# Kernel optimization log

Measured on AMD Instinct MI355X. Metric: run time of the kernel, lower is better.

The kernel has to match this reference:

```python
import jax, jax.numpy as jnp
import numpy as np

FACTOR = 0.5  # matches init_kwargs factor


def setup_inputs() -> dict:
    key = jax.random.key(0)
    k1, k2 = jax.random.split(key)
    E, D, N = 1600000, 32, 100000
    edge_data = jax.random.normal(k1, (E, D), dtype=jnp.float32)
    edge_dst = jax.random.randint(k2, (E,), 0, N, dtype=jnp.int64)
    return {"edge_data": edge_data, "edge_dst": edge_dst, "num_nodes": N}


def reference(edge_data, edge_dst, num_nodes):
    # EdgewiseReduce.forward: optional scalar premultiply, then scatter-sum
    # edge features into per-node bins by destination index.
    scaled = edge_data * FACTOR                     # [E, D]
    out = jax.ops.segment_sum(scaled, edge_dst, num_segments=num_nodes)  # [N, D]
    return out
```

## Files before the change

### kernel.cpp

```cpp
#include <hip/hip_runtime.h>
#include <hip/hip_bf16.h>


#define D 32
#define FACTOR 0.5f
#define BSHIFT 7
#define BNODES (1 << BSHIFT)
#define CAPSHIFT 12
#define CAP (1 << CAPSHIFT)

__global__ void init_kernel(int* __restrict__ cursor, int* __restrict__ ovf_count,
                            int nb) {
  int i = blockIdx.x * blockDim.x + threadIdx.x;
  if (i == 0) *ovf_count = 0;
  if (i < nb) cursor[i] = i << CAPSHIFT;
}

__global__ void scatter_kernel(const int* __restrict__ dst, int* __restrict__ gcursor,
                               int* __restrict__ order, int2* __restrict__ ovf,
                               int* __restrict__ ovf_count, int E, int N, int nb,
                               int chunk) {
  extern __shared__ int sm[];
  int* lhist = sm;
  int* lcur = sm + nb;
  int lo = blockIdx.x * chunk;
  int hiE = min(lo + chunk, E);
  const int4* dst4 = (const int4*)dst;

  for (int i = threadIdx.x; i < nb; i += blockDim.x) lhist[i] = 0;
  __syncthreads();

  int lo4 = lo >> 2;
  int full4 = (hiE - lo) >> 2;
  for (int i = threadIdx.x; i < full4; i += blockDim.x) {
    int4 v = dst4[lo4 + i];
    if ((unsigned)v.x < (unsigned)N) atomicAdd(&lhist[v.x >> BSHIFT], 1);
    if ((unsigned)v.y < (unsigned)N) atomicAdd(&lhist[v.y >> BSHIFT], 1);
    if ((unsigned)v.z < (unsigned)N) atomicAdd(&lhist[v.z >> BSHIFT], 1);
    if ((unsigned)v.w < (unsigned)N) atomicAdd(&lhist[v.w >> BSHIFT], 1);
  }
  int tb = lo + (full4 << 2) + threadIdx.x;
  if (tb < hiE) {
    int d = dst[tb];
    if ((unsigned)d < (unsigned)N) atomicAdd(&lhist[d >> BSHIFT], 1);
  }
  __syncthreads();

  for (int i = threadIdx.x; i < nb; i += blockDim.x) {
    int c = lhist[i];
    lcur[i] = c ? atomicAdd(&gcursor[i], c) : 0;
  }
  __syncthreads();

  #define EMIT(dd, ee)                                                        \
    if ((unsigned)(dd) < (unsigned)N) {                                       \
      int bkt = (dd) >> BSHIFT;                                               \
      int pos = atomicAdd(&lcur[bkt], 1);                                     \
      if (pos < ((bkt + 1) << CAPSHIFT)) {                                    \
        order[pos] = ((ee) << BSHIFT) | ((dd) & (BNODES - 1));                \
      } else {                                                                \
        int op = atomicAdd(ovf_count, 1);                                     \
        ovf[op] = make_int2((ee), (dd));                                      \
      }                                                                       \
    }

  for (int i = threadIdx.x; i < full4; i += blockDim.x) {
    int e = lo + (i << 2);
    int4 v = dst4[lo4 + i];
    EMIT(v.x, e + 0)
    EMIT(v.y, e + 1)
    EMIT(v.z, e + 2)
    EMIT(v.w, e + 3)
  }
  if (tb < hiE) {
    int d = dst[tb];
    EMIT(d, tb)
  }
  #undef EMIT
}

#define K4_THREADS 512
__global__ __launch_bounds__(K4_THREADS)
void gather_kernel(const float4* __restrict__ data, const int* __restrict__ order,
                   const int* __restrict__ cursor, float4* __restrict__ out,
                   int N) {
  __shared__ int ids[CAP];
  __shared__ int sorted[CAP];
  __shared__ int hist[BNODES];
  __shared__ int offs[BNODES];
  __shared__ int cur[BNODES];

  const int b = blockIdx.x;
  const int base = b << CAPSHIFT;
  int cnt = cursor[b] - base;
  if (cnt > CAP) cnt = CAP;
  const int lo = b << BSHIFT;
  const int tid = threadIdx.x;
  const int grp = tid >> 2;
  const int ln = tid & 3;

  for (int i = tid; i < BNODES; i += K4_THREADS) hist[i] = 0;
  __syncthreads();
  for (int i = tid; i < cnt; i += K4_THREADS) {
    int v = order[base + i];
    ids[i] = v;
    atomicAdd(&hist[v & (BNODES - 1)], 1);
  }
  __syncthreads();

  if (tid < 64) {
    int c0 = hist[2 * tid], c1 = hist[2 * tid + 1];
    int s = c0 + c1;
    int sc = s;
    #pragma unroll
    for (int off = 1; off < 64; off <<= 1) {
      int t = __shfl_up(sc, off);
      if (tid >= off) sc += t;
    }
    int bs = sc - s;
    offs[2 * tid] = bs + c0;
    offs[2 * tid + 1] = bs + c0 + c1;
    cur[2 * tid] = bs;
    cur[2 * tid + 1] = bs + c0;
  }
  __syncthreads();

  for (int i = tid; i < cnt; i += K4_THREADS) {
    int v = ids[i];
    sorted[atomicAdd(&cur[v & (BNODES - 1)], 1)] = v;
  }
  __syncthreads();

  float4 acc0 = make_float4(0.f, 0.f, 0.f, 0.f);
  float4 acc1 = make_float4(0.f, 0.f, 0.f, 0.f);
  int e_ = offs[grp];
  int i = e_ - hist[grp];
  for (; i + 3 < e_; i += 4) {
    int r0 = sorted[i] >> BSHIFT;
    int r1 = sorted[i + 1] >> BSHIFT;
    int r2 = sorted[i + 2] >> BSHIFT;
    int r3 = sorted[i + 3] >> BSHIFT;
    const float4* p0 = data + (size_t)r0 * 8 + ln * 2;
    const float4* p1 = data + (size_t)r1 * 8 + ln * 2;
    const float4* p2 = data + (size_t)r2 * 8 + ln * 2;
    const float4* p3 = data + (size_t)r3 * 8 + ln * 2;
    float4 x0 = p0[0], y0 = p0[1];
    float4 x1 = p1[0], y1 = p1[1];
    float4 x2 = p2[0], y2 = p2[1];
    float4 x3 = p3[0], y3 = p3[1];
    acc0.x += x0.x + x1.x + x2.x + x3.x;
    acc0.y += x0.y + x1.y + x2.y + x3.y;
    acc0.z += x0.z + x1.z + x2.z + x3.z;
    acc0.w += x0.w + x1.w + x2.w + x3.w;
    acc1.x += y0.x + y1.x + y2.x + y3.x;
    acc1.y += y0.y + y1.y + y2.y + y3.y;
    acc1.z += y0.z + y1.z + y2.z + y3.z;
    acc1.w += y0.w + y1.w + y2.w + y3.w;
  }
  for (; i < e_; ++i) {
    int r0 = sorted[i] >> BSHIFT;
    const float4* p0 = data + (size_t)r0 * 8 + ln * 2;
    float4 x0 = p0[0], y0 = p0[1];
    acc0.x += x0.x; acc0.y += x0.y; acc0.z += x0.z; acc0.w += x0.w;
    acc1.x += y0.x; acc1.y += y0.y; acc1.z += y0.z; acc1.w += y0.w;
  }

  int node = lo + grp;
  if (node < N) {
    float4 o0, o1;
    o0.x = acc0.x * FACTOR; o0.y = acc0.y * FACTOR;
    o0.z = acc0.z * FACTOR; o0.w = acc0.w * FACTOR;
    o1.x = acc1.x * FACTOR; o1.y = acc1.y * FACTOR;
    o1.z = acc1.z * FACTOR; o1.w = acc1.w * FACTOR;
    out[(size_t)node * 8 + ln * 2] = o0;
    out[(size_t)node * 8 + ln * 2 + 1] = o1;
  }
}

__global__ void overflow_kernel(const float4* __restrict__ data,
                                const int2* __restrict__ ovf,
                                const int* __restrict__ ovf_count,
                                float* __restrict__ out) {
  int cnt = *ovf_count;
  for (int i = blockIdx.x * blockDim.x + threadIdx.x; i < cnt * 8;
       i += gridDim.x * blockDim.x) {
    int k = i >> 3, q = i & 7;
    int2 ed = ovf[k];
    float4 v = data[(size_t)ed.x * 8 + q];
    float* p = out + (size_t)ed.y * D + q * 4;
    unsafeAtomicAdd(p + 0, v.x * FACTOR);
    unsafeAtomicAdd(p + 1, v.y * FACTOR);
    unsafeAtomicAdd(p + 2, v.z * FACTOR);
    unsafeAtomicAdd(p + 3, v.w * FACTOR);
  }
}

__global__ void atomic_kernel(const float4* __restrict__ edge_data,
                              const int* __restrict__ edge_dst,
                              float* __restrict__ out, int E, int N) {
  int tid = blockIdx.x * blockDim.x + threadIdx.x;
  int e = tid >> 3;
  int q = tid & 7;
  if (e >= E) return;
  int dst = edge_dst[e];
  if (dst < 0 || dst >= N) return;
  float4 v = edge_data[(size_t)e * 8 + q];
  float* p = out + (size_t)dst * D + q * 4;
  unsafeAtomicAdd(p + 0, v.x * FACTOR);
  unsafeAtomicAdd(p + 1, v.y * FACTOR);
  unsafeAtomicAdd(p + 2, v.z * FACTOR);
  unsafeAtomicAdd(p + 3, v.w * FACTOR);
}

extern "C" void kernel_launch(void* const* d_in, const int* in_sizes, int n_in,
                              void* d_out, int out_size, void* d_ws, size_t ws_size,
                              hipStream_t stream) {
  const float4* edge_data = (const float4*)d_in[0];
  const int* edge_dst = (const int*)d_in[1];

  int E = in_sizes[1];
  int N = out_size / D;

  int nb = (N + BNODES - 1) >> BSHIFT;
  size_t ofs_order = 4 + (size_t)nb;
  ofs_order = (ofs_order + 1) & ~(size_t)1;
  size_t ofs_ovf = ofs_order + (size_t)nb * CAP;
  ofs_ovf = (ofs_ovf + 1) & ~(size_t)1;
  size_t need = (ofs_ovf + (size_t)2 * E) * sizeof(int);
  bool pack_ok = ((long long)E << BSHIFT) < (1ll << 31) &&
                 (((long long)nb << CAPSHIFT) < (1ll << 31));

  if (ws_size < need || !pack_ok) {
    float* out = (float*)d_out;
    hipMemsetAsync(d_out, 0, (size_t)out_size * sizeof(float), stream);
    int total = E * 8;
    atomic_kernel<<<(total + 255) / 256, 256, 0, stream>>>(edge_data, edge_dst, out, E, N);
    return;
  }

  int* ws = (int*)d_ws;
  int* ovf_count = ws;
  int* cursor = ws + 4;
  int* order = ws + ofs_order;
  int2* ovf = (int2*)(ws + ofs_ovf);

  init_kernel<<<(nb + 1023) / 1024, 1024, 0, stream>>>(cursor, ovf_count, nb);

  int nblk = 128;
  int chunk = ((E + nblk - 1) / nblk + 3) & ~3;
  size_t lds = (size_t)2 * nb * sizeof(int);
  scatter_kernel<<<nblk, 256, lds, stream>>>(edge_dst, cursor, order, ovf,
                                             ovf_count, E, N, nb, chunk);

  gather_kernel<<<nb, K4_THREADS, 0, stream>>>(
      edge_data, order, cursor, (float4*)d_out, N);

  overflow_kernel<<<32, 256, 0, stream>>>(edge_data, ovf, ovf_count, (float*)d_out);
}
```

Baseline: 329.7 us.

## Balance gather work by splitting sorted edges evenly across groups with LDS flush

The gather kernel now gives each 4-thread group an equal contiguous slice of the bucket's sorted edge list instead of one node's edges. Partial sums are flushed into a shared-memory accumulator with LDS atomics at node boundaries, and the result is then scaled and written out. This targets load imbalance from varying node degrees within a block. In exchange it adds LDS atomics, extra per-edge boundary checks and another barrier, and it reuses the ids buffer as the accumulator.

```diff
diff --git a/kernel.cpp b/kernel.cpp
--- a/kernel.cpp
+++ b/kernel.cpp
@@ -84,16 +84,17 @@
 void gather_kernel(const float4* __restrict__ data, const int* __restrict__ order,
                    const int* __restrict__ cursor, float4* __restrict__ out,
                    int N) {
+  __shared__ int sorted[CAP];
   __shared__ int ids[CAP];
-  __shared__ int sorted[CAP];
   __shared__ int hist[BNODES];
-  __shared__ int offs[BNODES];
+  __shared__ int endo[BNODES];
   __shared__ int cur[BNODES];
 
   const int b = blockIdx.x;
   const int base = b << CAPSHIFT;
   int cnt = cursor[b] - base;
   if (cnt > CAP) cnt = CAP;
+  if (cnt < 0) cnt = 0;
   const int lo = b << BSHIFT;
   const int tid = threadIdx.x;
   const int grp = tid >> 2;
@@ -118,8 +119,8 @@
       if (tid >= off) sc += t;
     }
     int bs = sc - s;
-    offs[2 * tid] = bs + c0;
-    offs[2 * tid + 1] = bs + c0 + c1;
+    endo[2 * tid] = bs + c0;
+    endo[2 * tid + 1] = bs + c0 + c1;
     cur[2 * tid] = bs;
     cur[2 * tid + 1] = bs + c0;
   }
@@ -131,49 +132,75 @@
   }
   __syncthreads();
 
-  float4 acc0 = make_float4(0.f, 0.f, 0.f, 0.f);
-  float4 acc1 = make_float4(0.f, 0.f, 0.f, 0.f);
-  int e_ = offs[grp];
-  int i = e_ - hist[grp];
-  for (; i + 3 < e_; i += 4) {
-    int r0 = sorted[i] >> BSHIFT;
-    int r1 = sorted[i + 1] >> BSHIFT;
-    int r2 = sorted[i + 2] >> BSHIFT;
-    int r3 = sorted[i + 3] >> BSHIFT;
-    const float4* p0 = data + (size_t)r0 * 8 + ln * 2;
-    const float4* p1 = data + (size_t)r1 * 8 + ln * 2;
-    const float4* p2 = data + (size_t)r2 * 8 + ln * 2;
-    const float4* p3 = data + (size_t)r3 * 8 + ln * 2;
+  float* accf = (float*)ids;
+  for (int i = tid; i < BNODES * D; i += K4_THREADS) accf[i] = 0.f;
+  __syncthreads();
+
+  const int W = (cnt + BNODES - 1) >> BSHIFT;
+  const int i0 = grp * W;
+  const int i1 = min(i0 + W, cnt);
+
+  float4 a0 = make_float4(0.f, 0.f, 0.f, 0.f);
+  float4 a1 = make_float4(0.f, 0.f, 0.f, 0.f);
+
+  #define FLUSH(nd)                                                           \
+    {                                                                         \
+      float* fp = accf + ((nd) << 5) + (ln << 3);                             \
+      atomicAdd(fp + 0, a0.x); atomicAdd(fp + 1, a0.y);                       \
+      atomicAdd(fp + 2, a0.z); atomicAdd(fp + 3, a0.w);                       \
+      atomicAdd(fp + 4, a1.x); atomicAdd(fp + 5, a1.y);                       \
+      atomicAdd(fp + 6, a1.z); atomicAdd(fp + 7, a1.w);                       \
+      a0 = make_float4(0.f, 0.f, 0.f, 0.f);                                   \
+      a1 = make_float4(0.f, 0.f, 0.f, 0.f);                                   \
+    }
+
+  int j = i0;
+  for (; j + 3 < i1; j += 4) {
+    int v0 = sorted[j], v1 = sorted[j + 1], v2 = sorted[j + 2], v3 = sorted[j + 3];
+    const float4* p0 = data + (size_t)(v0 >> BSHIFT) * 8 + ln * 2;
+    const float4* p1 = data + (size_t)(v1 >> BSHIFT) * 8 + ln * 2;
+    const float4* p2 = data + (size_t)(v2 >> BSHIFT) * 8 + ln * 2;
+    const float4* p3 = data + (size_t)(v3 >> BSHIFT) * 8 + ln * 2;
     float4 x0 = p0[0], y0 = p0[1];
     float4 x1 = p1[0], y1 = p1[1];
     float4 x2 = p2[0], y2 = p2[1];
     float4 x3 = p3[0], y3 = p3[1];
-    acc0.x += x0.x + x1.x + x2.x + x3.x;
-    acc0.y += x0.y + x1.y + x2.y + x3.y;
-    acc0.z += x0.z + x1.z + x2.z + x3.z;
-    acc0.w += x0.w + x1.w + x2.w + x3.w;
-    acc1.x += y0.x + y1.x + y2.x + y3.x;
-    acc1.y += y0.y + y1.y + y2.y + y3.y;
-    acc1.z += y0.z + y1.z + y2.z + y3.z;
-    acc1.w += y0.w + y1.w + y2.w + y3.w;
-  }
-  for (; i < e_; ++i) {
-    int r0 = sorted[i] >> BSHIFT;
-    const float4* p0 = data + (size_t)r0 * 8 + ln * 2;
-    float4 x0 = p0[0], y0 = p0[1];
-    acc0.x += x0.x; acc0.y += x0.y; acc0.z += x0.z; acc0.w += x0.w;
-    acc1.x += y0.x; acc1.y += y0.y; acc1.z += y0.z; acc1.w += y0.w;
-  }
-
-  int node = lo + grp;
-  if (node < N) {
-    float4 o0, o1;
-    o0.x = acc0.x * FACTOR; o0.y = acc0.y * FACTOR;
-    o0.z = acc0.z * FACTOR; o0.w = acc0.w * FACTOR;
-    o1.x = acc1.x * FACTOR; o1.y = acc1.y * FACTOR;
-    o1.z = acc1.z * FACTOR; o1.w = acc1.w * FACTOR;
-    out[(size_t)node * 8 + ln * 2] = o0;
-    out[(size_t)node * 8 + ln * 2 + 1] = o1;
+    a0.x += x0.x; a0.y += x0.y; a0.z += x0.z; a0.w += x0.w;
+    a1.x += y0.x; a1.y += y0.y; a1.z += y0.z; a1.w += y0.w;
+    { int nd = v0 & (BNODES - 1); if (j + 1 == endo[nd]) FLUSH(nd); }
+    a0.x += x1.x; a0.y += x1.y; a0.z += x1.z; a0.w += x1.w;
+    a1.x += y1.x; a1.y += y1.y; a1.z += y1.z; a1.w += y1.w;
+    { int nd = v1 & (BNODES - 1); if (j + 2 == endo[nd]) FLUSH(nd); }
+    a0.x += x2.x; a0.y += x2.y; a0.z += x2.z; a0.w += x2.w;
+    a1.x += y2.x; a1.y += y2.y; a1.z += y2.z; a1.w += y2.w;
+    { int nd = v2 & (BNODES - 1); if (j + 3 == endo[nd]) FLUSH(nd); }
+    a0.x += x3.x; a0.y += x3.y; a0.z += x3.z; a0.w += x3.w;
+    a1.x += y3.x; a1.y += y3.y; a1.z += y3.z; a1.w += y3.w;
+    { int nd = v3 & (BNODES - 1); if (j + 4 == endo[nd]) FLUSH(nd); }
+  }
+  for (; j < i1; ++j) {
+    int v = sorted[j];
+    const float4* p = data + (size_t)(v >> BSHIFT) * 8 + ln * 2;
+    float4 x = p[0], y = p[1];
+    a0.x += x.x; a0.y += x.y; a0.z += x.z; a0.w += x.w;
+    a1.x += y.x; a1.y += y.y; a1.z += y.z; a1.w += y.w;
+    { int nd = v & (BNODES - 1); if (j + 1 == endo[nd]) FLUSH(nd); }
+  }
+  if (i1 > i0) {
+    int nd = sorted[i1 - 1] & (BNODES - 1);
+    if (i1 != endo[nd]) FLUSH(nd);
+  }
+  #undef FLUSH
+  __syncthreads();
+
+  const float4* accv = (const float4*)accf;
+  for (int i = tid; i < (BNODES * D) / 4; i += K4_THREADS) {
+    int node = lo + (i >> 3);
+    if (node < N) {
+      float4 v = accv[i];
+      v.x *= FACTOR; v.y *= FACTOR; v.z *= FACTOR; v.w *= FACTOR;
+      out[(size_t)node * 8 + (i & 7)] = v;
+    }
   }
 }
 
```

Result: no change. 334.7 us (+1.5%).

## Split bucket scatter across many small blocks holding indices in registers

Applied to the files above, without the earlier changes.

The scatter pass now launches one 512-thread block per 4096 edges instead of 128 large blocks that each loop over a long chunk. Each thread keeps its two int4 index loads in registers between the histogram and emit phases, so the indices are read from global memory once. The init kernel is replaced by a memset, with bucket base offsets folded into the local cursor. The cost is about 390 blocks that each clear and walk a histogram of roughly 782 buckets, plus many more global cursor atomics spread across blocks.

```diff
diff --git a/kernel.cpp b/kernel.cpp
--- a/kernel.cpp
+++ b/kernel.cpp
@@ -9,46 +9,52 @@
 #define CAPSHIFT 12
 #define CAP (1 << CAPSHIFT)
 
-__global__ void init_kernel(int* __restrict__ cursor, int* __restrict__ ovf_count,
-                            int nb) {
-  int i = blockIdx.x * blockDim.x + threadIdx.x;
-  if (i == 0) *ovf_count = 0;
-  if (i < nb) cursor[i] = i << CAPSHIFT;
-}
-
-__global__ void scatter_kernel(const int* __restrict__ dst, int* __restrict__ gcursor,
-                               int* __restrict__ order, int2* __restrict__ ovf,
-                               int* __restrict__ ovf_count, int E, int N, int nb,
-                               int chunk) {
+#define S_THREADS 512
+#define S_PER_T 2
+__global__ __launch_bounds__(S_THREADS)
+void scatter_kernel(const int* __restrict__ dst, int* __restrict__ gcursor,
+                    int* __restrict__ order, int2* __restrict__ ovf,
+                    int* __restrict__ ovf_count, int E, int N, int nb) {
   extern __shared__ int sm[];
   int* lhist = sm;
   int* lcur = sm + nb;
-  int lo = blockIdx.x * chunk;
-  int hiE = min(lo + chunk, E);
   const int4* dst4 = (const int4*)dst;
-
-  for (int i = threadIdx.x; i < nb; i += blockDim.x) lhist[i] = 0;
-  __syncthreads();
-
-  int lo4 = lo >> 2;
-  int full4 = (hiE - lo) >> 2;
-  for (int i = threadIdx.x; i < full4; i += blockDim.x) {
-    int4 v = dst4[lo4 + i];
-    if ((unsigned)v.x < (unsigned)N) atomicAdd(&lhist[v.x >> BSHIFT], 1);
-    if ((unsigned)v.y < (unsigned)N) atomicAdd(&lhist[v.y >> BSHIFT], 1);
-    if ((unsigned)v.z < (unsigned)N) atomicAdd(&lhist[v.z >> BSHIFT], 1);
-    if ((unsigned)v.w < (unsigned)N) atomicAdd(&lhist[v.w >> BSHIFT], 1);
-  }
-  int tb = lo + (full4 << 2) + threadIdx.x;
-  if (tb < hiE) {
-    int d = dst[tb];
-    if ((unsigned)d < (unsigned)N) atomicAdd(&lhist[d >> BSHIFT], 1);
-  }
-  __syncthreads();
-
-  for (int i = threadIdx.x; i < nb; i += blockDim.x) {
+  const int n4 = E >> 2;
+  const int base4 = blockIdx.x * (S_THREADS * S_PER_T);
+  const int i4a = base4 + threadIdx.x;
+  const int i4b = i4a + S_THREADS;
+  const bool tail_block = (blockIdx.x == gridDim.x - 1);
+
+  for (int i = threadIdx.x; i < nb; i += S_THREADS) lhist[i] = 0;
+  __syncthreads();
+
+  int4 va, vb;
+  bool ha = (i4a < n4), hb = (i4b < n4);
+  if (ha) {
+    va = dst4[i4a];
+    if ((unsigned)va.x < (unsigned)N) atomicAdd(&lhist[va.x >> BSHIFT], 1);
+    if ((unsigned)va.y < (unsigned)N) atomicAdd(&lhist[va.y >> BSHIFT], 1);
+    if ((unsigned)va.z < (unsigned)N) atomicAdd(&lhist[va.z >> BSHIFT], 1);
+    if ((unsigned)va.w < (unsigned)N) atomicAdd(&lhist[va.w >> BSHIFT], 1);
+  }
+  if (hb) {
+    vb = dst4[i4b];
+    if ((unsigned)vb.x < (unsigned)N) atomicAdd(&lhist[vb.x >> BSHIFT], 1);
+    if ((unsigned)vb.y < (unsigned)N) atomicAdd(&lhist[vb.y >> BSHIFT], 1);
+    if ((unsigned)vb.z < (unsigned)N) atomicAdd(&lhist[vb.z >> BSHIFT], 1);
+    if ((unsigned)vb.w < (unsigned)N) atomicAdd(&lhist[vb.w >> BSHIFT], 1);
+  }
+  if (tail_block) {
+    for (int e = (n4 << 2) + threadIdx.x; e < E; e += S_THREADS) {
+      int d = dst[e];
+      if ((unsigned)d < (unsigned)N) atomicAdd(&lhist[d >> BSHIFT], 1);
+    }
+  }
+  __syncthreads();
+
+  for (int i = threadIdx.x; i < nb; i += S_THREADS) {
     int c = lhist[i];
-    lcur[i] = c ? atomicAdd(&gcursor[i], c) : 0;
+    lcur[i] = (i << CAPSHIFT) + (c ? atomicAdd(&gcursor[i], c) : 0);
   }
   __syncthreads();
 
@@ -64,17 +70,25 @@
       }                                                                       \
     }
 
-  for (int i = threadIdx.x; i < full4; i += blockDim.x) {
-    int e = lo + (i << 2);
-    int4 v = dst4[lo4 + i];
-    EMIT(v.x, e + 0)
-    EMIT(v.y, e + 1)
-    EMIT(v.z, e + 2)
-    EMIT(v.w, e + 3)
-  }
-  if (tb < hiE) {
-    int d = dst[tb];
-    EMIT(d, tb)
+  if (ha) {
+    int e = i4a << 2;
+    EMIT(va.x, e + 0)
+    EMIT(va.y, e + 1)
+    EMIT(va.z, e + 2)
+    EMIT(va.w, e + 3)
+  }
+  if (hb) {
+    int e = i4b << 2;
+    EMIT(vb.x, e + 0)
+    EMIT(vb.y, e + 1)
+    EMIT(vb.z, e + 2)
+    EMIT(vb.w, e + 3)
+  }
+  if (tail_block) {
+    for (int e = (n4 << 2) + threadIdx.x; e < E; e += S_THREADS) {
+      int d = dst[e];
+      EMIT(d, e)
+    }
   }
   #undef EMIT
 }
@@ -92,8 +106,9 @@
 
   const int b = blockIdx.x;
   const int base = b << CAPSHIFT;
-  int cnt = cursor[b] - base;
+  int cnt = cursor[b];
   if (cnt > CAP) cnt = CAP;
+  if (cnt < 0) cnt = 0;
   const int lo = b << BSHIFT;
   const int tid = threadIdx.x;
   const int grp = tid >> 2;
@@ -244,13 +259,14 @@
   int* order = ws + ofs_order;
   int2* ovf = (int2*)(ws + ofs_ovf);
 
-  init_kernel<<<(nb + 1023) / 1024, 1024, 0, stream>>>(cursor, ovf_count, nb);
-
-  int nblk = 128;
-  int chunk = ((E + nblk - 1) / nblk + 3) & ~3;
+  hipMemsetAsync(ws, 0, (4 + (size_t)nb) * sizeof(int), stream);
+
+  int epb = S_THREADS * S_PER_T * 4;
+  int nblk = (E + epb - 1) / epb;
+  if (nblk < 1) nblk = 1;
   size_t lds = (size_t)2 * nb * sizeof(int);
-  scatter_kernel<<<nblk, 256, lds, stream>>>(edge_dst, cursor, order, ovf,
-                                             ovf_count, E, N, nb, chunk);
+  scatter_kernel<<<nblk, S_THREADS, lds, stream>>>(edge_dst, cursor, order, ovf,
+                                                   ovf_count, E, N, nb);
 
   gather_kernel<<<nb, K4_THREADS, 0, stream>>>(
       edge_data, order, cursor, (float4*)d_out, N);
```

Result: no change. 328.2 us (-0.4%).
